# Kernel tuning notes

Measured on AMD Instinct MI355X. Metric: run time of the kernel, lower is better.

## Reference

```python
import jax, jax.numpy as jnp
import numpy as np

TEMPERATURE = 0.1


def setup_inputs() -> dict:
    key = jax.random.key(0)
    k1, k2 = jax.random.split(key)
    B, D = 4096, 128
    z_i = jax.random.normal(k1, (B, D), dtype=jnp.float32)
    z_j = jax.random.normal(k2, (B, D), dtype=jnp.float32)
    return {"z_i": z_i, "z_j": z_j}


def reference(z_i, z_j):
    B = z_i.shape[0]
    n = 2 * B
    z = jnp.concatenate([z_i, z_j], axis=0)            # [2B, D]
    sim = jnp.matmul(z, z.T) / TEMPERATURE             # [2B, 2B]
    # positives: diag(sim, +B) and diag(sim, -B)
    pos = jnp.concatenate([jnp.diagonal(sim, B), jnp.diagonal(sim, -B)])[:, None]  # [2B, 1]
    # negatives: sim with diagonal removed, row-wise -> [2B, 2B-1]
    # strided trick equivalent to sim[~eye].reshape(n, n-1)
    neg = sim.ravel()[:-1].reshape(n - 1, n + 1)[:, 1:].reshape(n, n - 1)
    logits = jnp.concatenate([pos, neg], axis=1)       # [2B, 2B]
    # cross-entropy with labels all zero (positive in column 0)
    loss = jnp.mean(jax.nn.logsumexp(logits, axis=1) - logits[:, 0])
    return loss
```

## Files before the change

### kernel.cpp

```cpp
#include <hip/hip_runtime.h>
#include <stdint.h>

#define N_TOT  8192
#define BHALF  4096
#define DDIM   128
#define NSPLIT 8

typedef short bf16x8 __attribute__((ext_vector_type(8)));
typedef float f32x4  __attribute__((ext_vector_type(4)));

__device__ __forceinline__ float ex2(float x) { return __builtin_amdgcn_exp2f(x); }

__device__ __forceinline__ unsigned short f2bf(float f) {
    uint32_t u = __builtin_bit_cast(uint32_t, f);
    u += 0x7fff + ((u >> 16) & 1);
    return (unsigned short)(u >> 16);
}

__global__ void k_cast(const float* __restrict__ zi, const float* __restrict__ zj,
                       unsigned short* __restrict__ zb) {
    const float c = 3.798282440185f;
    int t = blockIdx.x * blockDim.x + threadIdx.x;
    int e = t * 4;
    int row = e >> 7;
    const float* src = (row < BHALF) ? (zi + e) : (zj + (e - BHALF * DDIM));
    float4 v = *reinterpret_cast<const float4*>(src);
    ushort4 o;
    o.x = f2bf(v.x * c); o.y = f2bf(v.y * c);
    o.z = f2bf(v.z * c); o.w = f2bf(v.w * c);
    *reinterpret_cast<ushort4*>(zb + e) = o;
}

__global__ void k_pos(const float* __restrict__ zi, const float* __restrict__ zj,
                      float* __restrict__ pos) {
    int wid  = (blockIdx.x * blockDim.x + threadIdx.x) >> 6;
    int lane = threadIdx.x & 63;
    const float* a = zi + wid * DDIM;
    const float* b = zj + wid * DDIM;
    float p = a[lane] * b[lane] + a[lane + 64] * b[lane + 64];
    #pragma unroll
    for (int m = 32; m; m >>= 1) p += __shfl_xor(p, m, 64);
    if (lane == 0) { pos[wid] = 10.f * p; pos[wid + BHALF] = 10.f * p; }
}

__launch_bounds__(256, 2)
__global__ void k_main(const unsigned short* __restrict__ zb,
                       float* __restrict__ pm, float* __restrict__ pl) {
    __shared__ unsigned short lds[64 * 136];
    const int tid  = threadIdx.x;
    const int w    = tid >> 6, lane = tid & 63;
    const int q    = lane >> 4, ln = lane & 15;
    const int rb   = blockIdx.x >> 3, cs = blockIdx.x & 7;
    const int rowBase = rb * 256 + w * 64;
    const int colBase = cs * 1024;

    bf16x8 afr[4][4];
    #pragma unroll
    for (int s = 0; s < 4; ++s) {
        const unsigned short* p = zb + (rowBase + s * 16 + ln) * DDIM + q * 8;
        #pragma unroll
        for (int kc = 0; kc < 4; ++kc)
            afr[s][kc] = *reinterpret_cast<const bf16x8*>(p + kc * 32);
    }

    float m[4][4], l[4][4];
    #pragma unroll
    for (int s = 0; s < 4; ++s)
        #pragma unroll
        for (int r = 0; r < 4; ++r) { m[s][r] = -1e38f; l[s][r] = 0.f; }

    for (int ch = 0; ch < 16; ++ch) {
        #pragma unroll
        for (int it = 0; it < 4; ++it) {
            int idx = it * 256 + tid;
            int col = idx >> 4, part = idx & 15;
            const uint4* g = reinterpret_cast<const uint4*>(
                zb + (colBase + ch * 64 + col) * DDIM + part * 8);
            *reinterpret_cast<uint4*>(&lds[col * 136 + part * 8]) = *g;
        }
        __syncthreads();

        for (int ct = 0; ct < 4; ++ct) {
            bf16x8 bfr[4];
            const unsigned short* bp = &lds[(ct * 16 + ln) * 136 + q * 8];
            #pragma unroll
            for (int kc = 0; kc < 4; ++kc)
                bfr[kc] = *reinterpret_cast<const bf16x8*>(bp + kc * 32);
            const int colTile = colBase + ch * 64 + ct * 16;

            #pragma unroll
            for (int s = 0; s < 4; ++s) {
                f32x4 acc = {0.f, 0.f, 0.f, 0.f};
                #pragma unroll
                for (int kc = 0; kc < 4; ++kc)
                    acc = __builtin_amdgcn_mfma_f32_16x16x32_bf16(
                        afr[s][kc], bfr[kc], acc, 0, 0, 0);
                if (colTile == rowBase + s * 16) {
                    #pragma unroll
                    for (int r = 0; r < 4; ++r)
                        if (ln == q * 4 + r) acc[r] = -__builtin_inff();
                }
                #pragma unroll
                for (int r = 0; r < 4; ++r) {
                    float t  = acc[r];
                    float mo = m[s][r];
                    float mn = fmaxf(mo, t);
                    float pv = ex2(t - mn);
                    float sc = ex2(mo - mn);
                    l[s][r] = l[s][r] * sc + pv;
                    m[s][r] = mn;
                }
            }
        }
        __syncthreads();
    }

    #pragma unroll
    for (int s = 0; s < 4; ++s) {
        #pragma unroll
        for (int r = 0; r < 4; ++r) {
            float mm = m[s][r], ll = l[s][r];
            #pragma unroll
            for (int msk = 1; msk < 16; msk <<= 1) {
                float om = __shfl_xor(mm, msk, 64);
                float ol = __shfl_xor(ll, msk, 64);
                float mn = fmaxf(mm, om);
                ll = ll * ex2(mm - mn) + ol * ex2(om - mn);
                mm = mn;
            }
            if (ln == 0) {
                int row = rowBase + s * 16 + q * 4 + r;
                pm[cs * N_TOT + row] = mm;
                pl[cs * N_TOT + row] = ll;
            }
        }
    }
}

__global__ void k_finish(const float* __restrict__ pm, const float* __restrict__ pl,
                         const float* __restrict__ pos, float* __restrict__ partial) {
    int row = blockIdx.x * 256 + threadIdx.x;
    float p  = pos[row];
    float tp = p * 1.4426950408889634f;
    float mm[NSPLIT];
    float M = tp;
    #pragma unroll
    for (int j = 0; j < NSPLIT; ++j) {
        mm[j] = pm[j * N_TOT + row];
        M = fmaxf(M, mm[j]);
    }
    float S = ex2(tp - M);
    #pragma unroll
    for (int j = 0; j < NSPLIT; ++j)
        S += pl[j * N_TOT + row] * ex2(mm[j] - M);
    float lse = (M + __log2f(S)) * 0.6931471805599453f;
    float li  = lse - p;
    #pragma unroll
    for (int msk = 32; msk; msk >>= 1) li += __shfl_xor(li, msk, 64);
    __shared__ float red[4];
    if ((threadIdx.x & 63) == 0) red[threadIdx.x >> 6] = li;
    __syncthreads();
    if (threadIdx.x == 0)
        partial[blockIdx.x] = red[0] + red[1] + red[2] + red[3];
}

__global__ void k_sum(const float* __restrict__ partial, float* __restrict__ out) {
    int lane = threadIdx.x & 63;
    float v = (lane < 32) ? partial[lane] : 0.f;
    #pragma unroll
    for (int msk = 32; msk; msk >>= 1) v += __shfl_xor(v, msk, 64);
    if (lane == 0) out[0] = v * (1.f / 8192.f);
}

extern "C" void kernel_launch(void* const* d_in, const int* in_sizes, int n_in,
                              void* d_out, int out_size, void* d_ws, size_t ws_size,
                              hipStream_t stream) {
    const float* zi = (const float*)d_in[0];
    const float* zj = (const float*)d_in[1];
    float* out = (float*)d_out;
    char* ws = (char*)d_ws;

    unsigned short* zb  = (unsigned short*)ws;
    float* pos          = (float*)(ws + 2u * 1024 * 1024);
    float* pm           = (float*)(ws + 2u * 1024 * 1024 + 32 * 1024);
    float* pl           = pm + NSPLIT * N_TOT;
    float* partial      = pl + NSPLIT * N_TOT;

    hipLaunchKernelGGL(k_cast,   dim3(1024), dim3(256), 0, stream, zi, zj, zb);
    hipLaunchKernelGGL(k_pos,    dim3(1024), dim3(256), 0, stream, zi, zj, pos);
    hipLaunchKernelGGL(k_main,   dim3(256),  dim3(256), 0, stream, zb, pm, pl);
    hipLaunchKernelGGL(k_finish, dim3(32),   dim3(256), 0, stream, pm, pl, pos, partial);
    hipLaunchKernelGGL(k_sum,    dim3(1),    dim3(64),  0, stream, partial, out);
}
```

Measured before the change: 105.0 us.

## Split columns 32 ways, fuse cast with positives, swizzle LDS, pair MFMA tiles

Raises the column split from 8 to 32, so k_main launches 1024 blocks instead of 256 and fills the GPU better. Each block now runs 4 chunks instead of 16, and occupancy is set to 3 blocks per CU. The cast and positive-pair kernels are merged into one prep kernel, which drops a launch and a second read of the inputs. LDS padding is replaced with an XOR swizzle, and two column tiles are processed per step, sharing one max/rescale across both. The costs are 4x more partial m/l traffic into k_finish and a per-block A-fragment reload that is now amortized over fewer columns.

```diff
diff --git a/kernel.cpp b/kernel.cpp
--- a/kernel.cpp
+++ b/kernel.cpp
@@ -4,7 +4,7 @@
 #define N_TOT  8192
 #define BHALF  4096
 #define DDIM   128
-#define NSPLIT 8
+#define NSPLIT 32
 
 typedef short bf16x8 __attribute__((ext_vector_type(8)));
 typedef float f32x4  __attribute__((ext_vector_type(4)));
@@ -17,42 +17,34 @@
     return (unsigned short)(u >> 16);
 }
 
-__global__ void k_cast(const float* __restrict__ zi, const float* __restrict__ zj,
-                       unsigned short* __restrict__ zb) {
+__global__ void k_prep(const float* __restrict__ zi, const float* __restrict__ zj,
+                       unsigned short* __restrict__ zb, float* __restrict__ pos) {
     const float c = 3.798282440185f;
-    int t = blockIdx.x * blockDim.x + threadIdx.x;
-    int e = t * 4;
-    int row = e >> 7;
-    const float* src = (row < BHALF) ? (zi + e) : (zj + (e - BHALF * DDIM));
-    float4 v = *reinterpret_cast<const float4*>(src);
-    ushort4 o;
-    o.x = f2bf(v.x * c); o.y = f2bf(v.y * c);
-    o.z = f2bf(v.z * c); o.w = f2bf(v.w * c);
-    *reinterpret_cast<ushort4*>(zb + e) = o;
-}
-
-__global__ void k_pos(const float* __restrict__ zi, const float* __restrict__ zj,
-                      float* __restrict__ pos) {
-    int wid  = (blockIdx.x * blockDim.x + threadIdx.x) >> 6;
+    int i    = blockIdx.x * 4 + (threadIdx.x >> 6);
     int lane = threadIdx.x & 63;
-    const float* a = zi + wid * DDIM;
-    const float* b = zj + wid * DDIM;
-    float p = a[lane] * b[lane] + a[lane + 64] * b[lane + 64];
+    const float2 a = *reinterpret_cast<const float2*>(zi + i * DDIM + lane * 2);
+    const float2 b = *reinterpret_cast<const float2*>(zj + i * DDIM + lane * 2);
+    ushort2 oa, ob;
+    oa.x = f2bf(a.x * c); oa.y = f2bf(a.y * c);
+    ob.x = f2bf(b.x * c); ob.y = f2bf(b.y * c);
+    *reinterpret_cast<ushort2*>(zb + i * DDIM + lane * 2) = oa;
+    *reinterpret_cast<ushort2*>(zb + (i + BHALF) * DDIM + lane * 2) = ob;
+    float p = a.x * b.x + a.y * b.y;
     #pragma unroll
     for (int m = 32; m; m >>= 1) p += __shfl_xor(p, m, 64);
-    if (lane == 0) { pos[wid] = 10.f * p; pos[wid + BHALF] = 10.f * p; }
-}
-
-__launch_bounds__(256, 2)
+    if (lane == 0) { pos[i] = 10.f * p; pos[i + BHALF] = 10.f * p; }
+}
+
+__launch_bounds__(256, 3)
 __global__ void k_main(const unsigned short* __restrict__ zb,
                        float* __restrict__ pm, float* __restrict__ pl) {
-    __shared__ unsigned short lds[64 * 136];
+    __shared__ unsigned short lds[64 * 128];
     const int tid  = threadIdx.x;
     const int w    = tid >> 6, lane = tid & 63;
     const int q    = lane >> 4, ln = lane & 15;
-    const int rb   = blockIdx.x >> 3, cs = blockIdx.x & 7;
+    const int rb   = blockIdx.x >> 5, cs = blockIdx.x & 31;
     const int rowBase = rb * 256 + w * 64;
-    const int colBase = cs * 1024;
+    const int colBase = cs * 256;
 
     bf16x8 afr[4][4];
     #pragma unroll
@@ -69,45 +61,62 @@
         #pragma unroll
         for (int r = 0; r < 4; ++r) { m[s][r] = -1e38f; l[s][r] = 0.f; }
 
-    for (int ch = 0; ch < 16; ++ch) {
+    for (int ch = 0; ch < 4; ++ch) {
         #pragma unroll
         for (int it = 0; it < 4; ++it) {
-            int idx = it * 256 + tid;
-            int col = idx >> 4, part = idx & 15;
-            const uint4* g = reinterpret_cast<const uint4*>(
-                zb + (colBase + ch * 64 + col) * DDIM + part * 8);
-            *reinterpret_cast<uint4*>(&lds[col * 136 + part * 8]) = *g;
+            int idx  = it * 256 + tid;
+            int col  = idx >> 4, g = idx & 15;
+            int slot = g ^ (col & 7);
+            const uint4* gp = reinterpret_cast<const uint4*>(
+                zb + (colBase + ch * 64 + col) * DDIM + g * 8);
+            *reinterpret_cast<uint4*>(&lds[col * 128 + slot * 8]) = *gp;
         }
         __syncthreads();
 
-        for (int ct = 0; ct < 4; ++ct) {
-            bf16x8 bfr[4];
-            const unsigned short* bp = &lds[(ct * 16 + ln) * 136 + q * 8];
+        #pragma unroll
+        for (int ct2 = 0; ct2 < 2; ++ct2) {
+            bf16x8 bfr[2][4];
             #pragma unroll
-            for (int kc = 0; kc < 4; ++kc)
-                bfr[kc] = *reinterpret_cast<const bf16x8*>(bp + kc * 32);
-            const int colTile = colBase + ch * 64 + ct * 16;
+            for (int u = 0; u < 2; ++u) {
+                int ct = ct2 * 2 + u;
+                #pragma unroll
+                for (int kc = 0; kc < 4; ++kc) {
+                    int slot = (q + 4 * kc) ^ (ln & 7);
+                    bfr[u][kc] = *reinterpret_cast<const bf16x8*>(
+                        &lds[(ct * 16 + ln) * 128 + slot * 8]);
+                }
+            }
+            const int c0 = colBase + ch * 64 + ct2 * 32;
 
             #pragma unroll
             for (int s = 0; s < 4; ++s) {
-                f32x4 acc = {0.f, 0.f, 0.f, 0.f};
+                f32x4 a0 = {0.f, 0.f, 0.f, 0.f}, a1 = {0.f, 0.f, 0.f, 0.f};
                 #pragma unroll
-                for (int kc = 0; kc < 4; ++kc)
-                    acc = __builtin_amdgcn_mfma_f32_16x16x32_bf16(
-                        afr[s][kc], bfr[kc], acc, 0, 0, 0);
-                if (colTile == rowBase + s * 16) {
+                for (int kc = 0; kc < 4; ++kc) {
+                    a0 = __builtin_amdgcn_mfma_f32_16x16x32_bf16(
+                        afr[s][kc], bfr[0][kc], a0, 0, 0, 0);
+                    a1 = __builtin_amdgcn_mfma_f32_16x16x32_bf16(
+                        afr[s][kc], bfr[1][kc], a1, 0, 0, 0);
+                }
+                const int rowTile = rowBase + s * 16;
+                if (c0 == rowTile) {
                     #pragma unroll
                     for (int r = 0; r < 4; ++r)
-                        if (ln == q * 4 + r) acc[r] = -__builtin_inff();
+                        if (ln == q * 4 + r) a0[r] = -__builtin_inff();
+                } else if (c0 + 16 == rowTile) {
+                    #pragma unroll
+                    for (int r = 0; r < 4; ++r)
+                        if (ln == q * 4 + r) a1[r] = -__builtin_inff();
                 }
                 #pragma unroll
                 for (int r = 0; r < 4; ++r) {
-                    float t  = acc[r];
+                    float t0 = a0[r], t1 = a1[r];
                     float mo = m[s][r];
-                    float mn = fmaxf(mo, t);
-                    float pv = ex2(t - mn);
+                    float mn = fmaxf(fmaxf(t0, t1), mo);
                     float sc = ex2(mo - mn);
-                    l[s][r] = l[s][r] * sc + pv;
+                    float p0 = ex2(t0 - mn);
+                    float p1 = ex2(t1 - mn);
+                    l[s][r] = fmaf(l[s][r], sc, p0 + p1);
                     m[s][r] = mn;
                 }
             }
@@ -180,15 +189,14 @@
     float* out = (float*)d_out;
     char* ws = (char*)d_ws;
 
-    unsigned short* zb  = (unsigned short*)ws;
-    float* pos          = (float*)(ws + 2u * 1024 * 1024);
-    float* pm           = (float*)(ws + 2u * 1024 * 1024 + 32 * 1024);
-    float* pl           = pm + NSPLIT * N_TOT;
-    float* partial      = pl + NSPLIT * N_TOT;
-
-    hipLaunchKernelGGL(k_cast,   dim3(1024), dim3(256), 0, stream, zi, zj, zb);
-    hipLaunchKernelGGL(k_pos,    dim3(1024), dim3(256), 0, stream, zi, zj, pos);
-    hipLaunchKernelGGL(k_main,   dim3(256),  dim3(256), 0, stream, zb, pm, pl);
+    unsigned short* zb = (unsigned short*)ws;
+    float* pos         = (float*)(ws + (size_t)2 * 1024 * 1024);
+    float* pm          = pos + N_TOT;
+    float* pl          = pm + NSPLIT * N_TOT;
+    float* partial     = pl + NSPLIT * N_TOT;
+
+    hipLaunchKernelGGL(k_prep,   dim3(1024), dim3(256), 0, stream, zi, zj, zb, pos);
+    hipLaunchKernelGGL(k_main,   dim3(1024), dim3(256), 0, stream, zb, pm, pl);
     hipLaunchKernelGGL(k_finish, dim3(32),   dim3(256), 0, stream, pm, pl, pos, partial);
     hipLaunchKernelGGL(k_sum,    dim3(1),    dim3(64),  0, stream, partial, out);
 }
```

Result: slower. 121.7 us (+15.9%).
